# Optimization experiments

Hardware: AMD Instinct MI355X
Metric: run time of the kernel (lower is better)

The kernel has to match this reference:

```python
import jax, jax.numpy as jnp
import numpy as np

B, T, C = 4, 2048, 1024
H, DH = 16, 64  # num_heads, head_size; H*DH == C


def setup_inputs() -> dict:
    key = jax.random.key(0)
    ks = jax.random.split(key, 6)
    s = C ** -0.5
    x = jax.random.normal(ks[0], (B, T, C), dtype=jnp.float32)
    # per-head projection weights, stacked: [H, C, DH]
    Wq = jax.random.normal(ks[1], (H, C, DH), dtype=jnp.float32) * s
    Wk = jax.random.normal(ks[2], (H, C, DH), dtype=jnp.float32) * s
    Wv = jax.random.normal(ks[3], (H, C, DH), dtype=jnp.float32) * s
    # output projection (with bias, as nn.Linear default)
    Wo = jax.random.normal(ks[4], (C, C), dtype=jnp.float32) * s
    bo = jax.random.normal(ks[5], (C,), dtype=jnp.float32) * 0.01
    return {"x": x, "Wq": Wq, "Wk": Wk, "Wv": Wv, "Wo": Wo, "bo": bo}


def reference(x, Wq, Wk, Wv, Wo, bo):
    Bv, Tv, Cv = x.shape
    scale = DH ** -0.5
    # project to per-head q/k/v: [B, H, T, DH]
    q = jnp.einsum('btc,hcd->bhtd', x, Wq)
    k = jnp.einsum('btc,hcd->bhtd', x, Wk)
    v = jnp.einsum('btc,hcd->bhtd', x, Wv)
    # scaled scores [B, H, T, T] with causal mask
    scores = jnp.einsum('bhtd,bhsd->bhts', q, k) * scale
    causal = jnp.tril(jnp.ones((Tv, Tv), dtype=bool))
    scores = jnp.where(causal, scores, -jnp.inf)
    wei = jax.nn.softmax(scores, axis=-1)
    out = jnp.einsum('bhts,bhsd->bhtd', wei, v)
    # concat heads: [B, T, H*DH] == [B, T, C]
    out = out.transpose(0, 2, 1, 3).reshape(Bv, Tv, Cv)
    return out @ Wo.T + bo
```

## Files before the change

kernel.cpp:

```cpp
#include <hip/hip_runtime.h>
#include <stdint.h>

typedef unsigned short u16;
typedef __attribute__((ext_vector_type(8))) short short8;
typedef __attribute__((ext_vector_type(4))) float floatx4;

#define MFMA_BF16 __builtin_amdgcn_mfma_f32_16x16x32_bf16

#define BB 4
#define TT 2048
#define CC 1024
#define HH 16
#define DH 64
#define MM (BB * TT)
#define NQKV (3 * CC)

#define SOFTMAX_OFF 23.083120654223414f

__device__ __forceinline__ u16 f2bf(float f) {
  union { float f; uint32_t u; } un;
  un.f = f;
  uint32_t u = un.u;
  u += 0x7fffu + ((u >> 16) & 1u);
  return (u16)(u >> 16);
}

__device__ __forceinline__ uint32_t pk2(float a, float b) {
  return (uint32_t)f2bf(a) | ((uint32_t)f2bf(b) << 16);
}

__device__ __forceinline__ uint32_t pktrunc(float a, float b) {
  union { float f; uint32_t u; } ua, ub;
  ua.f = a; ub.f = b;
  return __builtin_amdgcn_perm(ub.u, ua.u, 0x07060302u);
}

__device__ __forceinline__ void gload_lds16(const u16* g, u16* l) {
  __builtin_amdgcn_global_load_lds(
      (const __attribute__((address_space(1))) unsigned int*)g,
      (__attribute__((address_space(3))) unsigned int*)l, 16, 0, 0);
}

__global__ __launch_bounds__(256) void convert_kernel(
    const float* __restrict__ x, const float* __restrict__ Wq,
    const float* __restrict__ Wk, const float* __restrict__ Wv,
    const float* __restrict__ Wo, u16* __restrict__ xb,
    u16* __restrict__ Wt, u16* __restrict__ Wob) {
  __shared__ float T[32][33];
  int bid = blockIdx.x, tid = threadIdx.x;
  if (bid < 8192) {
    int i = (bid * 256 + tid) * 4;
    float4 f = *(const float4*)(x + i);
    uint2 o = {pk2(f.x, f.y), pk2(f.z, f.w)};
    *(uint2*)(xb + i) = o;
  } else if (bid < 8192 + 3072) {
    int tb = bid - 8192;
    int sec = tb >> 10, rem = tb & 1023;
    int h = rem >> 6, sub = rem & 63, ct = sub >> 1, dt = sub & 1;
    const float* W = (sec == 0) ? Wq : (sec == 1) ? Wk : Wv;
    int tx = tid & 31, ty = tid >> 5;
#pragma unroll
    for (int p = 0; p < 4; ++p)
      T[ty + 8 * p][tx] =
          W[((size_t)h * CC + ct * 32 + ty + 8 * p) * DH + dt * 32 + tx];
    __syncthreads();
#pragma unroll
    for (int p = 0; p < 4; ++p) {
      int n = sec * 1024 + h * 64 + dt * 32 + ty + 8 * p;
      Wt[(size_t)n * CC + ct * 32 + tx] = f2bf(T[tx][ty + 8 * p]);
    }
  } else {
    int i = ((bid - 11264) * 256 + tid) * 4;
    float4 f = *(const float4*)(Wo + i);
    uint2 o = {pk2(f.x, f.y), pk2(f.z, f.w)};
    *(uint2*)(Wob + i) = o;
  }
}

template <int MODE>
__global__ __launch_bounds__(256) void gemm_bt(
    const u16* __restrict__ A, const u16* __restrict__ Bt, int M, int N, int K,
    u16* __restrict__ qout, u16* __restrict__ kout, u16* __restrict__ vout,
    float* __restrict__ out, const float* __restrict__ bias) {
  __shared__ u16 As[128][64];
  __shared__ u16 Bs[128][64];
  int tid = threadIdx.x;
  int lane = tid & 63, w = tid >> 6;
  int wm = w >> 1, wn = w & 1;
  int g = lane >> 4, c = lane & 15;
  int m0 = blockIdx.y * 128, n0 = blockIdx.x * 128;

  floatx4 acc[4][4];
#pragma unroll
  for (int i = 0; i < 4; ++i)
#pragma unroll
    for (int j = 0; j < 4; ++j) acc[i][j] = (floatx4){0.f, 0.f, 0.f, 0.f};

  int srow = 32 * w + (lane >> 3);
  int scol = (lane & 7) * 8;
  const u16* Ag = A + (size_t)(m0 + srow) * K + scol;
  const u16* Bg = Bt + (size_t)(n0 + srow) * K + scol;
  u16* AsB = &As[32 * w][0];
  u16* BsB = &Bs[32 * w][0];

  for (int k0 = 0; k0 < K; k0 += 64) {
    __syncthreads();
#pragma unroll
    for (int j = 0; j < 4; ++j)
      gload_lds16(Ag + k0 + (size_t)j * 8 * K, AsB + j * 512);
#pragma unroll
    for (int j = 0; j < 4; ++j)
      gload_lds16(Bg + k0 + (size_t)j * 8 * K, BsB + j * 512);
    __syncthreads();
#pragma unroll
    for (int kc = 0; kc < 2; ++kc) {
      short8 af[4], bfv[4];
#pragma unroll
      for (int mt = 0; mt < 4; ++mt)
        af[mt] = *(const short8*)(&As[wm * 64 + mt * 16 + c][kc * 32 + g * 8]);
#pragma unroll
      for (int nt = 0; nt < 4; ++nt)
        bfv[nt] = *(const short8*)(&Bs[wn * 64 + nt * 16 + c][kc * 32 + g * 8]);
#pragma unroll
      for (int mt = 0; mt < 4; ++mt)
#pragma unroll
        for (int nt = 0; nt < 4; ++nt)
          acc[mt][nt] = MFMA_BF16(af[mt], bfv[nt], acc[mt][nt], 0, 0, 0);
    }
  }

#pragma unroll
  for (int mt = 0; mt < 4; ++mt) {
#pragma unroll
    for (int nt = 0; nt < 4; ++nt) {
#pragma unroll
      for (int r = 0; r < 4; ++r) {
        int m = m0 + wm * 64 + mt * 16 + g * 4 + r;
        int n = n0 + wn * 64 + nt * 16 + c;
        float v = acc[mt][nt][r];
        if (MODE == 0) {
          int b = m >> 11, t = m & 2047;
          int sec = n >> 10, h = (n >> 6) & 15, d = n & 63;
          size_t idx = (((size_t)(b * HH + h)) * TT + t) * DH + d;
          if (sec == 0)
            qout[idx] = f2bf(v * 0.18033688011112042f);
          else if (sec == 1)
            kout[idx] = f2bf(v);
          else
            vout[idx] = f2bf(v);
        } else {
          out[(size_t)m * N + n] = v + bias[n];
        }
      }
    }
  }
}

__global__ __launch_bounds__(256) void vtrans(const u16* __restrict__ v,
                                              u16* __restrict__ vP) {
  __shared__ u16 Ld[64][72];
  int tile = blockIdx.x, bh = blockIdx.y, tid = threadIdx.x;
  int row = tid >> 2, col = (tid & 3) * 16;
  const u16* src = v + ((size_t)bh * TT + tile * 64 + row) * DH + col;
  *(uint4*)(&Ld[row][col]) = *(const uint4*)(src);
  *(uint4*)(&Ld[row][col + 8]) = *(const uint4*)(src + 8);
  __syncthreads();
  int d = tid >> 2, u0 = (tid & 3) * 16;
  union { u16 h[16]; uint4 q[2]; } o;
#pragma unroll
  for (int k = 0; k < 16; ++k) {
    int u = u0 + k;
    int s = ((u & 3) << 4) | (u >> 2);
    o.h[k] = Ld[s][d];
  }
  u16* dst = vP + ((size_t)(bh * DH + d)) * TT + tile * 64 + u0;
  *(uint4*)(dst) = o.q[0];
  *(uint4*)(dst + 8) = o.q[1];
}

__global__ __launch_bounds__(256, 4) void flash_attn(
    const u16* __restrict__ q, const u16* __restrict__ k,
    const u16* __restrict__ vP, u16* __restrict__ O) {
  __shared__ u16 Ks[64][72];
  __shared__ u16 Vs[64][72];
  __shared__ u16 Ps[4][32][72];

  int tid = threadIdx.x;
  int lane = tid & 63, w = tid >> 6;
  int g = lane >> 4, c = lane & 15;

  int id = blockIdx.y * 16 + blockIdx.x;
  int bh = id >> 4;
  int x = id & 15;
  int t0 = (((id >> 8) & 1) ? x : 15 - x) * 128;

  const u16* qb = q + (size_t)bh * TT * DH;
  const u16* kb = k + (size_t)bh * TT * DH;
  const u16* vb = vP + (size_t)bh * DH * TT;

  short8 qf[2][2];
#pragma unroll
  for (int mt = 0; mt < 2; ++mt) {
    int qrow = t0 + w * 32 + mt * 16 + c;
#pragma unroll
    for (int kc = 0; kc < 2; ++kc)
      qf[mt][kc] = *(const short8*)(qb + (size_t)qrow * DH + kc * 32 + g * 8);
  }

  floatx4 oacc[2][4];
#pragma unroll
  for (int mt = 0; mt < 2; ++mt)
#pragma unroll
    for (int nt = 0; nt < 4; ++nt) oacc[mt][nt] = (floatx4){0.f, 0.f, 0.f, 0.f};
  float lsum[2][4];
#pragma unroll
  for (int mt = 0; mt < 2; ++mt)
#pragma unroll
    for (int r = 0; r < 4; ++r) lsum[mt][r] = 0.f;

  int srow = tid >> 2, scol = (tid & 3) * 16;
  const u16* kbase = kb + (size_t)srow * DH + scol;
  const u16* vbase = vb + (size_t)srow * TT + scol;

  uint4 kr0 = *(const uint4*)(kbase);
  uint4 kr1 = *(const uint4*)(kbase + 8);
  uint4 vr0 = *(const uint4*)(vbase);
  uint4 vr1 = *(const uint4*)(vbase + 8);

  int niter = (t0 >> 6) + 2;
  int nfull = t0 >> 6;
  int wmax = t0 + w * 32 + 31;
  for (int it = 0; it < niter; ++it) {
    int s0 = it << 6;
    __syncthreads();
    *(uint4*)(&Ks[srow][scol]) = kr0;
    *(uint4*)(&Ks[srow][scol + 8]) = kr1;
    *(uint4*)(&Vs[srow][scol]) = vr0;
    *(uint4*)(&Vs[srow][scol + 8]) = vr1;
    __syncthreads();
    if (it + 1 < niter) {
      size_t koff = (size_t)((it + 1) << 6) * DH;
      int voff = (it + 1) << 6;
      kr0 = *(const uint4*)(kbase + koff);
      kr1 = *(const uint4*)(kbase + koff + 8);
      vr0 = *(const uint4*)(vbase + voff);
      vr1 = *(const uint4*)(vbase + voff + 8);
    }
    if (s0 > wmax) continue;
    bool masked = (it >= nfull);

    floatx4 z[2][4];
#pragma unroll
    for (int mt = 0; mt < 2; ++mt)
#pragma unroll
      for (int n = 0; n < 4; ++n) z[mt][n] = (floatx4){0.f, 0.f, 0.f, 0.f};
#pragma unroll
    for (int kc = 0; kc < 2; ++kc)
#pragma unroll
      for (int n = 0; n < 4; ++n) {
        short8 kf = *(const short8*)(&Ks[n * 16 + c][kc * 32 + g * 8]);
        z[0][n] = MFMA_BF16(qf[0][kc], kf, z[0][n], 0, 0, 0);
        z[1][n] = MFMA_BF16(qf[1][kc], kf, z[1][n], 0, 0, 0);
      }

#pragma unroll
    for (int mt = 0; mt < 2; ++mt) {
      int qr = t0 + w * 32 + mt * 16 + g * 4;
#pragma unroll
      for (int r = 0; r < 4; ++r) {
        float p0 = exp2f(z[mt][0][r] - SOFTMAX_OFF);
        float p1 = exp2f(z[mt][1][r] - SOFTMAX_OFF);
        float p2 = exp2f(z[mt][2][r] - SOFTMAX_OFF);
        float p3 = exp2f(z[mt][3][r] - SOFTMAX_OFF);
        if (masked) {
          if (s0 + c > qr + r) p0 = 0.f;
          if (s0 + 16 + c > qr + r) p1 = 0.f;
          if (s0 + 32 + c > qr + r) p2 = 0.f;
          if (s0 + 48 + c > qr + r) p3 = 0.f;
        }
        lsum[mt][r] += (p0 + p1) + (p2 + p3);
        uint2 pk = {pktrunc(p0, p1), pktrunc(p2, p3)};
        *(uint2*)(&Ps[w][mt * 16 + g * 4 + r][4 * c]) = pk;
      }
    }

#pragma unroll
    for (int kc = 0; kc < 2; ++kc) {
      short8 pf0 = *(const short8*)(&Ps[w][c][kc * 32 + g * 8]);
      short8 pf1 = *(const short8*)(&Ps[w][16 + c][kc * 32 + g * 8]);
#pragma unroll
      for (int nt = 0; nt < 4; ++nt) {
        short8 vf = *(const short8*)(&Vs[nt * 16 + c][kc * 32 + g * 8]);
        oacc[0][nt] = MFMA_BF16(pf0, vf, oacc[0][nt], 0, 0, 0);
        oacc[1][nt] = MFMA_BF16(pf1, vf, oacc[1][nt], 0, 0, 0);
      }
    }
  }

  int b = bh >> 4, h = bh & 15;
#pragma unroll
  for (int mt = 0; mt < 2; ++mt) {
#pragma unroll
    for (int r = 0; r < 4; ++r) {
      float l = lsum[mt][r];
      l += __shfl_xor(l, 1);
      l += __shfl_xor(l, 2);
      l += __shfl_xor(l, 4);
      l += __shfl_xor(l, 8);
      lsum[mt][r] = 1.f / l;
    }
#pragma unroll
    for (int nt = 0; nt < 4; ++nt)
#pragma unroll
      for (int r = 0; r < 4; ++r) {
        int trow = t0 + w * 32 + mt * 16 + g * 4 + r;
        float ov = oacc[mt][nt][r] * lsum[mt][r];
        O[((size_t)b * TT + trow) * CC + h * DH + nt * 16 + c] = f2bf(ov);
      }
  }
}

extern "C" void kernel_launch(void* const* d_in, const int* in_sizes, int n_in,
                              void* d_out, int out_size, void* d_ws,
                              size_t ws_size, hipStream_t stream) {
  const float* x = (const float*)d_in[0];
  const float* Wq = (const float*)d_in[1];
  const float* Wk = (const float*)d_in[2];
  const float* Wv = (const float*)d_in[3];
  const float* Wo = (const float*)d_in[4];
  const float* bo = (const float*)d_in[5];
  float* out = (float*)d_out;

  u16* ws = (u16*)d_ws;
  u16* xb = ws;
  u16* Wt = xb + 8388608;
  u16* Wob = Wt + 3145728;
  u16* qw = Wob + 1048576;
  u16* kw = qw + 8388608;
  u16* vw = kw + 8388608;
  u16* vP = vw + 8388608;
  u16* Ow = xb;

  convert_kernel<<<12288, 256, 0, stream>>>(x, Wq, Wk, Wv, Wo, xb, Wt, Wob);

  gemm_bt<0><<<dim3(NQKV / 128, MM / 128), 256, 0, stream>>>(
      xb, Wt, MM, NQKV, CC, qw, kw, vw, nullptr, nullptr);

  vtrans<<<dim3(TT / 64, BB * HH), 256, 0, stream>>>(vw, vP);

  flash_attn<<<dim3(TT / 128, BB * HH), 256, 0, stream>>>(qw, kw, vP, Ow);

  gemm_bt<1><<<dim3(CC / 128, MM / 128), 256, 0, stream>>>(
      Ow, Wob, MM, CC, CC, nullptr, nullptr, nullptr, out, bo);
}
```

Baseline: 314.2 us.

## Stage GEMM epilogues through LDS and fuse V transpose into QKV GEMM

Both GEMM epilogues now stage accumulators through shared memory so each thread writes 16-byte vectors instead of scattered 2-byte or 4-byte stores. The QKV GEMM writes V directly in the permuted transposed layout that flash attention expects, which removes the separate vtrans kernel and its extra read and write of V. The cost is extra LDS round trips and barriers in the epilogue, and a 32-element per-thread temp array for the V transpose that may raise register pressure.

```diff
diff --git a/kernel.cpp b/kernel.cpp
--- a/kernel.cpp
+++ b/kernel.cpp
@@ -82,8 +82,9 @@
     const u16* __restrict__ A, const u16* __restrict__ Bt, int M, int N, int K,
     u16* __restrict__ qout, u16* __restrict__ kout, u16* __restrict__ vout,
     float* __restrict__ out, const float* __restrict__ bias) {
-  __shared__ u16 As[128][64];
-  __shared__ u16 Bs[128][64];
+  __shared__ __align__(16) u16 SMEM[16384];
+  u16* As = SMEM;
+  u16* Bs = SMEM + 8192;
   int tid = threadIdx.x;
   int lane = tid & 63, w = tid >> 6;
   int wm = w >> 1, wn = w & 1;
@@ -100,8 +101,8 @@
   int scol = (lane & 7) * 8;
   const u16* Ag = A + (size_t)(m0 + srow) * K + scol;
   const u16* Bg = Bt + (size_t)(n0 + srow) * K + scol;
-  u16* AsB = &As[32 * w][0];
-  u16* BsB = &Bs[32 * w][0];
+  u16* AsB = As + 32 * w * 64;
+  u16* BsB = Bs + 32 * w * 64;
 
   for (int k0 = 0; k0 < K; k0 += 64) {
     __syncthreads();
@@ -117,10 +118,10 @@
       short8 af[4], bfv[4];
 #pragma unroll
       for (int mt = 0; mt < 4; ++mt)
-        af[mt] = *(const short8*)(&As[wm * 64 + mt * 16 + c][kc * 32 + g * 8]);
+        af[mt] = *(const short8*)(As + (wm * 64 + mt * 16 + c) * 64 + kc * 32 + g * 8);
 #pragma unroll
       for (int nt = 0; nt < 4; ++nt)
-        bfv[nt] = *(const short8*)(&Bs[wn * 64 + nt * 16 + c][kc * 32 + g * 8]);
+        bfv[nt] = *(const short8*)(Bs + (wn * 64 + nt * 16 + c) * 64 + kc * 32 + g * 8);
 #pragma unroll
       for (int mt = 0; mt < 4; ++mt)
 #pragma unroll
@@ -129,53 +130,87 @@
     }
   }
 
-#pragma unroll
-  for (int mt = 0; mt < 4; ++mt) {
-#pragma unroll
-    for (int nt = 0; nt < 4; ++nt) {
-#pragma unroll
-      for (int r = 0; r < 4; ++r) {
-        int m = m0 + wm * 64 + mt * 16 + g * 4 + r;
-        int n = n0 + wn * 64 + nt * 16 + c;
-        float v = acc[mt][nt][r];
-        if (MODE == 0) {
-          int b = m >> 11, t = m & 2047;
-          int sec = n >> 10, h = (n >> 6) & 15, d = n & 63;
-          size_t idx = (((size_t)(b * HH + h)) * TT + t) * DH + d;
-          if (sec == 0)
-            qout[idx] = f2bf(v * 0.18033688011112042f);
-          else if (sec == 1)
-            kout[idx] = f2bf(v);
-          else
-            vout[idx] = f2bf(v);
-        } else {
-          out[(size_t)m * N + n] = v + bias[n];
+  if (MODE == 0) {
+    const int CST = 136;
+    u16* Cs = SMEM;
+    int sec = n0 >> 10;
+    int h0 = (n0 >> 6) & 15;
+    int b = m0 >> 11;
+    int tbase = m0 & 2047;
+    u16* dst = (sec == 0) ? qout : (sec == 1) ? kout : vout;
+#pragma unroll
+    for (int p = 0; p < 2; ++p) {
+      __syncthreads();
+      if (wm == p) {
+#pragma unroll
+        for (int mt = 0; mt < 4; ++mt)
+#pragma unroll
+          for (int nt = 0; nt < 4; ++nt)
+#pragma unroll
+            for (int r = 0; r < 4; ++r) {
+              float v = acc[mt][nt][r];
+              if (sec == 0) v *= 0.18033688011112042f;
+              Cs[(mt * 16 + g * 4 + r) * CST + wn * 64 + nt * 16 + c] = f2bf(v);
+            }
+      }
+      __syncthreads();
+      if (sec < 2) {
+        int row = tid >> 2, nc = (tid & 3) * 32;
+        int t = tbase + p * 64 + row;
+        int h = h0 + (nc >> 6), d0 = nc & 63;
+        u16* dp = dst + (((size_t)(b * HH + h) * TT + t) * DH + d0);
+#pragma unroll
+        for (int j = 0; j < 4; ++j)
+          *(uint4*)(dp + j * 8) = *(const uint4*)(&Cs[row * CST + nc + j * 8]);
+      } else {
+        int d = tid >> 1, u0 = (tid & 1) * 32;
+        int h = h0 + (d >> 6), dd = d & 63;
+        int tile = (tbase >> 6) + p;
+        u16* dp = dst + (((size_t)(b * HH + h) * DH + dd) * TT + tile * 64 + u0);
+        u16 tmp[32];
+#pragma unroll
+        for (int i = 0; i < 32; ++i) {
+          int u = u0 + i;
+          int s = ((u & 3) << 4) | (u >> 2);
+          tmp[i] = Cs[s * CST + d];
         }
-      }
-    }
-  }
-}
-
-__global__ __launch_bounds__(256) void vtrans(const u16* __restrict__ v,
-                                              u16* __restrict__ vP) {
-  __shared__ u16 Ld[64][72];
-  int tile = blockIdx.x, bh = blockIdx.y, tid = threadIdx.x;
-  int row = tid >> 2, col = (tid & 3) * 16;
-  const u16* src = v + ((size_t)bh * TT + tile * 64 + row) * DH + col;
-  *(uint4*)(&Ld[row][col]) = *(const uint4*)(src);
-  *(uint4*)(&Ld[row][col + 8]) = *(const uint4*)(src + 8);
-  __syncthreads();
-  int d = tid >> 2, u0 = (tid & 3) * 16;
-  union { u16 h[16]; uint4 q[2]; } o;
-#pragma unroll
-  for (int k = 0; k < 16; ++k) {
-    int u = u0 + k;
-    int s = ((u & 3) << 4) | (u >> 2);
-    o.h[k] = Ld[s][d];
-  }
-  u16* dst = vP + ((size_t)(bh * DH + d)) * TT + tile * 64 + u0;
-  *(uint4*)(dst) = o.q[0];
-  *(uint4*)(dst + 8) = o.q[1];
+#pragma unroll
+        for (int j = 0; j < 4; ++j)
+          *(uint4*)(dp + j * 8) = *(const uint4*)(&tmp[j * 8]);
+      }
+    }
+  } else {
+    const int CSF = 132;
+    float* Csf = (float*)SMEM;
+    float4 bv[4];
+#pragma unroll
+    for (int j = 0; j < 4; ++j)
+      bv[j] = *(const float4*)(bias + n0 + (tid & 7) * 16 + j * 4);
+#pragma unroll
+    for (int p = 0; p < 4; ++p) {
+      __syncthreads();
+      if (wm == (p >> 1)) {
+        int mt0 = (p & 1) * 2;
+#pragma unroll
+        for (int mtl = 0; mtl < 2; ++mtl)
+#pragma unroll
+          for (int nt = 0; nt < 4; ++nt)
+#pragma unroll
+            for (int r = 0; r < 4; ++r)
+              Csf[(mtl * 16 + g * 4 + r) * CSF + wn * 64 + nt * 16 + c] =
+                  acc[mt0 + mtl][nt][r];
+      }
+      __syncthreads();
+      int row = tid >> 3, c0 = (tid & 7) * 16;
+      float* op = out + (size_t)(m0 + p * 32 + row) * N + n0 + c0;
+#pragma unroll
+      for (int j = 0; j < 4; ++j) {
+        float4 v = *(const float4*)(&Csf[row * CSF + c0 + j * 4]);
+        v.x += bv[j].x; v.y += bv[j].y; v.z += bv[j].z; v.w += bv[j].w;
+        *(float4*)(op + j * 4) = v;
+      }
+    }
+  }
 }
 
 __global__ __launch_bounds__(256, 4) void flash_attn(
@@ -337,16 +372,13 @@
   u16* Wob = Wt + 3145728;
   u16* qw = Wob + 1048576;
   u16* kw = qw + 8388608;
-  u16* vw = kw + 8388608;
-  u16* vP = vw + 8388608;
+  u16* vP = kw + 8388608;
   u16* Ow = xb;
 
   convert_kernel<<<12288, 256, 0, stream>>>(x, Wq, Wk, Wv, Wo, xb, Wt, Wob);
 
   gemm_bt<0><<<dim3(NQKV / 128, MM / 128), 256, 0, stream>>>(
-      xb, Wt, MM, NQKV, CC, qw, kw, vw, nullptr, nullptr);
-
-  vtrans<<<dim3(TT / 64, BB * HH), 256, 0, stream>>>(vw, vP);
+      xb, Wt, MM, NQKV, CC, qw, kw, vP, nullptr, nullptr);
 
   flash_attn<<<dim3(TT / 128, BB * HH), 256, 0, stream>>>(qw, kw, vP, Ow);
 
```

Result: no change. 317.3 us (+1.0%).
